# Optimization experiments

Measured on AMD Instinct MI355X. Metric: run time of the kernel, lower is better.

The kernel has to match this reference:

```python
import jax, jax.numpy as jnp
import numpy as np
import math

# gpt-oss style GQA dims
H, HKV, D = 64, 8, 64          # query heads, kv heads, head_dim
M = H // HKV                    # q_mult (queries per kv head)
D_MODEL = 2880
SLIDING_WINDOW = 128
SM_SCALE = 1.0 / math.sqrt(D)
NEG = -1e30


def _rope_cos_sin(T):
    # YaRN / NTK-by-parts rope (gpt-oss RotaryEmbedding) with
    # base=150000, initial_context_length=1024, scaling=32, alpha=1, beta=32
    base, init_ctx, scaling, alpha, beta = 150000.0, 1024.0, 32.0, 1.0, 32.0
    d_half = D // 2
    freq = base ** (np.arange(0, D, 2, dtype=np.float32) / D)
    concentration = 0.1 * math.log(scaling) + 1.0
    low = d_half * math.log(init_ctx / (beta * 2.0 * math.pi)) / math.log(base)
    high = d_half * math.log(init_ctx / (alpha * 2.0 * math.pi)) / math.log(base)
    ramp = np.clip((np.arange(d_half, dtype=np.float32) - low) / (high - low), 0.0, 1.0)
    inv_freq = ramp / (scaling * freq) + (1.0 - ramp) / freq  # interp<->extrap blend
    freqs = np.outer(np.arange(T, dtype=np.float32), inv_freq)  # (T, D/2)
    return (jnp.asarray(np.cos(freqs) * concentration),
            jnp.asarray(np.sin(freqs) * concentration))


def _apply_rope(x, cos, sin):
    # x[..., :D/2], x[..., D/2:] rotated pairwise; cos/sin broadcast over head dims
    x1, x2 = jnp.split(x, 2, axis=-1)
    return jnp.concatenate([x1 * cos - x2 * sin, x2 * cos + x1 * sin], axis=-1)


def setup_inputs() -> dict:
    key = jax.random.key(0)
    ks = jax.random.split(key, 6)
    x = jax.random.normal(ks[0], (1, 1536, D_MODEL), dtype=jnp.float32)
    qkv_dim = D * (H + 2 * HKV)
    W_qkv = jax.random.normal(ks[1], (D_MODEL, qkv_dim), dtype=jnp.float32) * 0.02
    b_qkv = jax.random.normal(ks[2], (qkv_dim,), dtype=jnp.float32) * 0.02
    W_out = jax.random.normal(ks[3], (H * D, D_MODEL), dtype=jnp.float32) * 0.02
    b_out = jax.random.normal(ks[4], (D_MODEL,), dtype=jnp.float32) * 0.02
    sinks = jax.random.normal(ks[5], (H,), dtype=jnp.float32) / math.sqrt(D)
    return {"x": x, "W_qkv": W_qkv, "b_qkv": b_qkv, "W_out": W_out,
            "b_out": b_out, "sinks": sinks}


def reference(x, W_qkv, b_qkv, W_out, b_out, sinks):
    B, T, _ = x.shape
    qkv = x @ W_qkv + b_qkv
    q = qkv[..., :H * D].reshape(B, T, HKV, M, D)
    k = qkv[..., H * D:(H + HKV) * D].reshape(B, T, HKV, D)
    v = qkv[..., (H + HKV) * D:].reshape(B, T, HKV, D)
    cos, sin = _rope_cos_sin(T)
    q = _apply_rope(q, cos[None, :, None, None, :], sin[None, :, None, None, :])
    k = _apply_rope(k, cos[None, :, None, :], sin[None, :, None, :])
    # GQA scores: (B, HKV, M, Tq, Tk)
    logits = jnp.einsum('bqhmd,bkhd->bhmqk', q, k) * SM_SCALE
    i = jnp.arange(T)[:, None]
    j = jnp.arange(T)[None, :]
    mask = (j <= i) & (j > i - SLIDING_WINDOW)  # causal + sliding window
    logits = jnp.where(mask[None, None, None], logits, NEG)
    m = jnp.max(logits, axis=-1, keepdims=True)
    e = jnp.exp(logits - m)
    # learned per-head sink logit folded into the softmax denominator
    exp_sink = jnp.exp(sinks.reshape(HKV, M)[None, :, :, None, None] - m)
    w = e / (jnp.sum(e, axis=-1, keepdims=True) + exp_sink)
    out = jnp.einsum('bhmqk,bkhd->bqhmd', w, v).reshape(B, T, H * D)
    return out @ W_out + b_out
```

## Files before the change

### kernel.cpp

```cpp
#include <hip/hip_runtime.h>

typedef __bf16 bf16_t;
typedef __bf16 bfrag8 __attribute__((ext_vector_type(8)));
typedef float f32x4 __attribute__((ext_vector_type(4)));

#define T_SEQ 1536
#define LDQKV 5120
#define SM_SCALE 0.125f
#define LOG2E 1.4426950408889634f

__device__ __forceinline__ unsigned short b2u(bf16_t h) {
  union { bf16_t h; unsigned short u; } c; c.h = h; return c.u;
}
__device__ __forceinline__ unsigned int pack2(float lo, float hi) {
  return (unsigned int)b2u((bf16_t)lo) | ((unsigned int)b2u((bf16_t)hi) << 16);
}
__device__ __forceinline__ void gload_lds16(const bf16_t* g, bf16_t* l) {
  __builtin_amdgcn_global_load_lds(
      (const __attribute__((address_space(1))) void*)g,
      (__attribute__((address_space(3))) void*)l, 16, 0, 0);
}

__global__ __launch_bounds__(256, 3)
void gemm_bt(const bf16_t* __restrict__ A, const bf16_t* __restrict__ Bt,
             const float* __restrict__ bias, void* __restrict__ C,
             int M, int N, int K, int out_mode) {
  __shared__ __align__(16) bf16_t As[128 * 64];
  __shared__ __align__(16) bf16_t Bs[128 * 64];
  const int tid = threadIdx.x;
  const int wave = tid >> 6;
  const int lane = tid & 63;
  const int g = lane >> 4;
  const int lm = lane & 15;

  const int NX = gridDim.x;
  const int nwg = NX * gridDim.y;
  const int orig = blockIdx.y * NX + blockIdx.x;
  const int qq = nwg >> 3, rr = nwg & 7;
  const int xcd = orig & 7, sidx = orig >> 3;
  const int swz = (xcd < rr ? xcd * (qq + 1) : rr * (qq + 1) + (xcd - rr) * qq) + sidx;
  const int n0 = (swz % NX) * 128;
  const int m0 = (swz / NX) * 128;

  const int tot = K >> 6;
  const int KS = gridDim.z;
  const int s = blockIdx.z;
  const int base = tot / KS, rem = tot % KS;
  const int ksteps = base + (s < rem ? 1 : 0);
  const int kbeg = s * base + (s < rem ? s : rem);

  const int wm = (wave >> 1) * 64;
  const int wn = (wave & 1) * 64;
  const int srow = lane >> 3;
  const int sseg = lane & 7;
  const int sswz = sseg ^ srow;

  const bf16_t* gA = A + (size_t)(m0 + wave * 32 + srow) * K + sswz * 8;
  const bf16_t* gB = Bt + (size_t)(n0 + wave * 32 + srow) * K + sswz * 8;
  bf16_t* lA = As + (wave * 32) * 64;
  bf16_t* lB = Bs + (wave * 32) * 64;

  const f32x4 fz = {0.f, 0.f, 0.f, 0.f};
  f32x4 acc[4][4];
#pragma unroll
  for (int i = 0; i < 4; ++i)
#pragma unroll
    for (int j = 0; j < 4; ++j) acc[i][j] = fz;

  const int lm7 = lm & 7;
  for (int t = 0; t < ksteps; ++t) {
    const int k0 = (kbeg + t) << 6;
#pragma unroll
    for (int it = 0; it < 4; ++it) {
      gload_lds16(gA + (size_t)(it * 8) * K + k0, lA + it * 8 * 64);
      gload_lds16(gB + (size_t)(it * 8) * K + k0, lB + it * 8 * 64);
    }
    __syncthreads();
#pragma unroll
    for (int ks = 0; ks < 2; ++ks) {
      bfrag8 af[4], bfr[4];
#pragma unroll
      for (int i = 0; i < 4; ++i) {
        const int cA = ((ks * 4 + g) ^ lm7) * 8;
        af[i]  = *(const bfrag8*)(As + (wm + i * 16 + lm) * 64 + cA);
        bfr[i] = *(const bfrag8*)(Bs + (wn + i * 16 + lm) * 64 + cA);
      }
#pragma unroll
      for (int i = 0; i < 4; ++i)
#pragma unroll
        for (int j = 0; j < 4; ++j)
          acc[i][j] = __builtin_amdgcn_mfma_f32_16x16x32_bf16(af[i], bfr[j],
                                                              acc[i][j], 0, 0, 0);
    }
    __syncthreads();
  }

  float* Cpart = (float*)C + (out_mode == 2 ? (size_t)s * M * N : 0);
#pragma unroll
  for (int j = 0; j < 4; ++j) {
    int n = n0 + wn + j * 16 + lm;
    if (n >= N) continue;
    float bv = (out_mode == 2) ? 0.f : bias[n];
#pragma unroll
    for (int i = 0; i < 4; ++i) {
      int mr = m0 + wm + i * 16 + g * 4;
#pragma unroll
      for (int r = 0; r < 4; ++r) {
        float v = acc[i][j][r] + bv;
        size_t off = (size_t)(mr + r) * N + n;
        if (out_mode == 1) ((bf16_t*)C)[off] = (bf16_t)v;
        else               Cpart[off] = v;
      }
    }
  }
}

__global__ __launch_bounds__(256)
void reduce_splits(const float* __restrict__ p, size_t MN,
                   const float* __restrict__ bias, int N,
                   void* __restrict__ dst, int out_bf16, int nsplit) {
  const size_t i4 = ((size_t)blockIdx.x * 256 + threadIdx.x) * 4;
  const int col = (int)(i4 % (size_t)N);
  f32x4 v = *(const f32x4*)(bias + col);
  for (int s = 0; s < nsplit; ++s) {
    f32x4 a = *(const f32x4*)(p + (size_t)s * MN + i4);
#pragma unroll
    for (int e = 0; e < 4; ++e) v[e] += a[e];
  }
  if (out_bf16) {
    uint2 w;
    w.x = pack2(v[0], v[1]);
    w.y = pack2(v[2], v[3]);
    *(uint2*)((bf16_t*)dst + i4) = w;
  } else {
    *(f32x4*)((float*)dst + i4) = v;
  }
}

__global__ __launch_bounds__(256)
void convert_x(const float* __restrict__ src, bf16_t* __restrict__ dst) {
  const int i8 = (blockIdx.x * 256 + threadIdx.x) * 8;
  f32x4 a = *(const f32x4*)(src + i8);
  f32x4 b = *(const f32x4*)(src + i8 + 4);
  uint4 w;
  w.x = pack2(a[0], a[1]);
  w.y = pack2(a[2], a[3]);
  w.z = pack2(b[0], b[1]);
  w.w = pack2(b[2], b[3]);
  *(uint4*)(dst + i8) = w;
}

__global__ __launch_bounds__(256)
void transpose_w(const float* __restrict__ src, bf16_t* __restrict__ dst,
                 int Ksrc, int Nsrc) {
  __shared__ bf16_t tile[32 * 33];
  const int t = threadIdx.x;
  const int r = t >> 3;
  const int c4 = (t & 7) * 4;
  const int n0 = blockIdx.x * 32;
  const int k0 = blockIdx.y * 32;
  f32x4 v = {0.f, 0.f, 0.f, 0.f};
  if (n0 + c4 < Nsrc)
    v = *(const f32x4*)(src + (size_t)(k0 + r) * Nsrc + n0 + c4);
#pragma unroll
  for (int e = 0; e < 4; ++e) tile[(c4 + e) * 33 + r] = (bf16_t)v[e];
  __syncthreads();
  uint2 w;
  w.x = pack2((float)tile[r * 33 + c4], (float)tile[r * 33 + c4 + 1]);
  w.y = pack2((float)tile[r * 33 + c4 + 2], (float)tile[r * 33 + c4 + 3]);
  *(uint2*)(dst + (size_t)(n0 + r) * Ksrc + k0 + c4) = w;
}

__global__ __launch_bounds__(256, 2)
void gemm_mfma(const void* __restrict__ A, const float* __restrict__ B,
               const float* __restrict__ bias, void* __restrict__ C,
               int M, int N, int K, int a_bf16, int out_bf16) {
  __shared__ __align__(16) bf16_t As[128 * 64];
  __shared__ __align__(16) bf16_t Bs[128 * 72];
  const int tid = threadIdx.x;
  const int wave = tid >> 6;
  const int lane = tid & 63;
  const int g = lane >> 4;
  const int lm = lane & 15;
  const int m0 = blockIdx.y * 128;
  const int n0 = blockIdx.x * 128;
  const int wm = (wave >> 1) * 64;
  const int wn = (wave & 1) * 64;
  const int sr = lane >> 3;
  const int seg = lane & 7;
  const int pairk = tid & 31;
  const int cg = tid >> 5;

  int cb = n0 + cg * 16;
  if (cb > N - 16) cb = N - 16;

  const f32x4 fz = {0.f, 0.f, 0.f, 0.f};
  f32x4 acc[4][4];
#pragma unroll
  for (int i = 0; i < 4; ++i)
#pragma unroll
    for (int j = 0; j < 4; ++j) acc[i][j] = fz;

  for (int k0 = 0; k0 < K; k0 += 64) {
    bfrag8 areg[4];
    if (a_bf16) {
#pragma unroll
      for (int it = 0; it < 4; ++it) {
        int ra = (wave * 4 + it) * 8 + sr;
        areg[it] = *(const bfrag8*)((const bf16_t*)A + (size_t)(m0 + ra) * K + k0 + seg * 8);
      }
    } else {
#pragma unroll
      for (int it = 0; it < 4; ++it) {
        int ra = (wave * 4 + it) * 8 + sr;
        const float* ga = (const float*)A + (size_t)(m0 + ra) * K + k0 + seg * 8;
        f32x4 a0 = *(const f32x4*)ga;
        f32x4 a1 = *(const f32x4*)(ga + 4);
#pragma unroll
        for (int e = 0; e < 4; ++e) {
          areg[it][e]     = (bf16_t)a0[e];
          areg[it][e + 4] = (bf16_t)a1[e];
        }
      }
    }
    int kk = 2 * pairk;
    unsigned int pk[16];
    {
      const float* b0 = B + (size_t)(k0 + kk) * N + cb;
      const float* b1 = B + (size_t)(k0 + kk + 1) * N + cb;
      f32x4 x0 = *(const f32x4*)(b0),     x1 = *(const f32x4*)(b0 + 4);
      f32x4 x2 = *(const f32x4*)(b0 + 8), x3 = *(const f32x4*)(b0 + 12);
      f32x4 y0 = *(const f32x4*)(b1),     y1 = *(const f32x4*)(b1 + 4);
      f32x4 y2 = *(const f32x4*)(b1 + 8), y3 = *(const f32x4*)(b1 + 12);
#pragma unroll
      for (int e = 0; e < 4; ++e) {
        pk[e]      = pack2(x0[e], y0[e]);
        pk[e + 4]  = pack2(x1[e], y1[e]);
        pk[e + 8]  = pack2(x2[e], y2[e]);
        pk[e + 12] = pack2(x3[e], y3[e]);
      }
    }
    __syncthreads();
#pragma unroll
    for (int it = 0; it < 4; ++it) {
      int ra = (wave * 4 + it) * 8 + sr;
      *(bfrag8*)(As + ra * 64 + seg * 8) = areg[it];
    }
#pragma unroll
    for (int n = 0; n < 16; ++n)
      *(unsigned int*)(Bs + (cg * 16 + n) * 72 + kk) = pk[n];
    __syncthreads();
#pragma unroll
    for (int ks = 0; ks < 2; ++ks) {
      bfrag8 af[4], bfr[4];
#pragma unroll
      for (int i = 0; i < 4; ++i) {
        af[i]  = *(const bfrag8*)(As + (wm + i * 16 + lm) * 64 + ks * 32 + g * 8);
        bfr[i] = *(const bfrag8*)(Bs + (wn + i * 16 + lm) * 72 + ks * 32 + g * 8);
      }
#pragma unroll
      for (int i = 0; i < 4; ++i)
#pragma unroll
        for (int j = 0; j < 4; ++j)
          acc[i][j] = __builtin_amdgcn_mfma_f32_16x16x32_bf16(af[i], bfr[j],
                                                              acc[i][j], 0, 0, 0);
    }
  }
#pragma unroll
  for (int j = 0; j < 4; ++j) {
    int n = n0 + wn + j * 16 + lm;
    if (n >= N) continue;
    float bv = bias[n];
#pragma unroll
    for (int i = 0; i < 4; ++i) {
      int mr = m0 + wm + i * 16 + g * 4;
#pragma unroll
      for (int r = 0; r < 4; ++r) {
        float v = acc[i][j][r] + bv;
        size_t off = (size_t)(mr + r) * N + n;
        if (out_bf16) ((bf16_t*)C)[off] = (bf16_t)v;
        else          ((float*)C)[off] = v;
      }
    }
  }
}

__global__ __launch_bounds__(256)
void rope_kernel(bf16_t* __restrict__ qkv) {
  int idx = blockIdx.x * 256 + threadIdx.x;
  int d = idx & 31;
  int rest = idx >> 5;
  int u = rest % 72;
  int t = rest / 72;
  if (t >= T_SEQ) return;
  int col = (u < 64) ? (u * 64) : (4096 + (u - 64) * 64);
  size_t off = (size_t)t * LDQKV + col + d;
  float x1 = (float)qkv[off];
  float x2 = (float)qkv[off + 32];
  const float lowv = 4.370846f;
  const float highv = 13.675927f;
  const float conc = 1.3465736f;
  float ramp = ((float)d - lowv) / (highv - lowv);
  ramp = fminf(fmaxf(ramp, 0.f), 1.f);
  float freq = exp2f((float)d * 0.53733134f);
  float inv_freq = ramp / (32.f * freq) + (1.f - ramp) / freq;
  float ang = (float)t * inv_freq;
  float c = cosf(ang) * conc;
  float s = sinf(ang) * conc;
  qkv[off]      = (bf16_t)(x1 * c - x2 * s);
  qkv[off + 32] = (bf16_t)(x2 * c + x1 * s);
}

__global__ __launch_bounds__(256, 2)
void attn_mfma(const bf16_t* __restrict__ qkv, const float* __restrict__ sinks,
               bf16_t* __restrict__ attno) {
  __shared__ __align__(16) bf16_t Vt[64 * 40];
  const int tid = threadIdx.x;
  const int wave = tid >> 6;
  const int lane = tid & 63;
  const int g = lane >> 4;
  const int lm = lane & 15;
  const int q0 = blockIdx.x * 32;
  const int kvh = blockIdx.y;
  const int jbase = q0 - 128;
  const int kt0 = (blockIdx.x < 4) ? (4 - blockIdx.x) : 0;

  bfrag8 qf[4][2];
#pragma unroll
  for (int nq = 0; nq < 4; ++nq) {
    const int h = 2 * wave + (nq >> 1);
    const int qr = q0 + (nq & 1) * 16 + lm;
    const bf16_t* qp = qkv + (size_t)qr * LDQKV + kvh * 512 + h * 64 + g * 8;
    qf[nq][0] = *(const bfrag8*)qp;
    qf[nq][1] = *(const bfrag8*)(qp + 32);
  }

  const f32x4 fz = {0.f, 0.f, 0.f, 0.f};
  f32x4 ot[4][4];
#pragma unroll
  for (int dt = 0; dt < 4; ++dt)
#pragma unroll
    for (int nq = 0; nq < 4; ++nq) ot[dt][nq] = fz;
  float mrow[4] = {-1e30f, -1e30f, -1e30f, -1e30f};
  float lrow[4] = {0.f, 0.f, 0.f, 0.f};

  const int vj = tid >> 3;
  const int vd = (tid & 7) * 8;

  for (int kt = kt0; kt < 5; ++kt) {
    const int ktb = jbase + kt * 32;
    __syncthreads();
    {
      bfrag8 v8 = *(const bfrag8*)(qkv + (size_t)(ktb + vj) * LDQKV + 4608 + kvh * 64 + vd);
#pragma unroll
      for (int e = 0; e < 8; ++e) Vt[(vd + e) * 40 + vj] = v8[e];
    }
    bfrag8 kf[2][2];
#pragma unroll
    for (int nk = 0; nk < 2; ++nk) {
      const bf16_t* kp = qkv + (size_t)(ktb + nk * 16 + lm) * LDQKV + 4096 + kvh * 64 + g * 8;
      kf[nk][0] = *(const bfrag8*)kp;
      kf[nk][1] = *(const bfrag8*)(kp + 32);
    }
    f32x4 st[2][4];
#pragma unroll
    for (int nk = 0; nk < 2; ++nk)
#pragma unroll
      for (int nq = 0; nq < 4; ++nq) st[nk][nq] = fz;
#pragma unroll
    for (int ks = 0; ks < 2; ++ks)
#pragma unroll
      for (int nk = 0; nk < 2; ++nk)
#pragma unroll
        for (int nq = 0; nq < 4; ++nq)
          st[nk][nq] = __builtin_amdgcn_mfma_f32_16x16x32_bf16(
              kf[nk][ks], qf[nq][ks], st[nk][nq], 0, 0, 0);

    bfrag8 paf[4];
#pragma unroll
    for (int nq = 0; nq < 4; ++nq) {
      const int q = q0 + (nq & 1) * 16 + lm;
      float sc[8];
      float pm = -1e30f;
#pragma unroll
      for (int nk = 0; nk < 2; ++nk)
#pragma unroll
        for (int r = 0; r < 4; ++r) {
          const int j = ktb + nk * 16 + g * 4 + r;
          const bool ok = (j <= q) && (j > q - 128);
          const float s = ok ? st[nk][nq][r] * (SM_SCALE * LOG2E) : -1e30f;
          sc[nk * 4 + r] = s;
          pm = fmaxf(pm, s);
        }
      pm = fmaxf(pm, __shfl_xor(pm, 16));
      pm = fmaxf(pm, __shfl_xor(pm, 32));
      const float mn = fmaxf(mrow[nq], pm);
      const float alpha = exp2f(mrow[nq] - mn);
      mrow[nq] = mn;
      float p[8];
      float ls = 0.f;
#pragma unroll
      for (int e = 0; e < 8; ++e) {
        p[e] = (sc[e] > -1e29f) ? exp2f(sc[e] - mn) : 0.f;
        ls += p[e];
      }
      lrow[nq] = lrow[nq] * alpha + ls;
#pragma unroll
      for (int dt = 0; dt < 4; ++dt) ot[dt][nq] *= alpha;
      unsigned pk00 = pack2(p[0], p[1]);
      unsigned pk01 = pack2(p[2], p[3]);
      unsigned pk10 = pack2(p[4], p[5]);
      unsigned pk11 = pack2(p[6], p[7]);
      const int srcA = ((g & 1) << 5) | lm;
      const int srcB = srcA + 16;
      unsigned a0 = __shfl(pk00, srcA), b0 = __shfl(pk10, srcA);
      unsigned a1 = __shfl(pk01, srcA), b1 = __shfl(pk11, srcA);
      unsigned a2 = __shfl(pk00, srcB), b2 = __shfl(pk10, srcB);
      unsigned a3 = __shfl(pk01, srcB), b3 = __shfl(pk11, srcB);
      const bool hiw = g >= 2;
      union { unsigned u[4]; bfrag8 f; } pa;
      pa.u[0] = hiw ? b0 : a0;
      pa.u[1] = hiw ? b1 : a1;
      pa.u[2] = hiw ? b2 : a2;
      pa.u[3] = hiw ? b3 : a3;
      paf[nq] = pa.f;
    }
    __syncthreads();
#pragma unroll
    for (int dt = 0; dt < 4; ++dt) {
      const bfrag8 vtf = *(const bfrag8*)(Vt + (dt * 16 + lm) * 40 + g * 8);
#pragma unroll
      for (int nq = 0; nq < 4; ++nq)
        ot[dt][nq] = __builtin_amdgcn_mfma_f32_16x16x32_bf16(
            vtf, paf[nq], ot[dt][nq], 0, 0, 0);
    }
  }

#pragma unroll
  for (int nq = 0; nq < 4; ++nq) {
    float lt = lrow[nq] + __shfl_xor(lrow[nq], 16);
    lt += __shfl_xor(lt, 32);
    const int h = 2 * wave + (nq >> 1);
    const float sk = sinks[kvh * 8 + h];
    const float inv = 1.f / (lt + exp2f(sk * LOG2E - mrow[nq]));
    const int q = q0 + (nq & 1) * 16 + lm;
    bf16_t* op = attno + (size_t)q * 4096 + kvh * 512 + h * 64;
#pragma unroll
    for (int dt = 0; dt < 4; ++dt) {
      const f32x4 o = ot[dt][nq];
      uint2 w;
      w.x = pack2(o[0] * inv, o[1] * inv);
      w.y = pack2(o[2] * inv, o[3] * inv);
      *(uint2*)(op + dt * 16 + g * 4) = w;
    }
  }
}

__global__ __launch_bounds__(256)
void sentinel_fill(float* __restrict__ out, int n) {
  int i = blockIdx.x * 256 + threadIdx.x;
  if (i < n) out[i] = 10000.0f;
}

extern "C" void kernel_launch(void* const* d_in, const int* in_sizes, int n_in,
                              void* d_out, int out_size, void* d_ws, size_t ws_size,
                              hipStream_t stream) {
  const float *x = nullptr, *Wqkv = nullptr, *bqkv = nullptr,
              *Wout = nullptr, *bout = nullptr, *sinks = nullptr;
  for (int i = 0; i < n_in; ++i) {
    switch (in_sizes[i]) {
      case 1536 * 2880:  x = (const float*)d_in[i]; break;
      case 2880 * 5120:  Wqkv = (const float*)d_in[i]; break;
      case 5120:         bqkv = (const float*)d_in[i]; break;
      case 4096 * 2880:  Wout = (const float*)d_in[i]; break;
      case 2880:         bout = (const float*)d_in[i]; break;
      case 64:           sinks = (const float*)d_in[i]; break;
      default: break;
    }
  }

  const size_t N_QKV  = (size_t)1536 * 5120;
  const size_t N_ATT  = (size_t)1536 * 4096;
  const size_t N_XB   = (size_t)1536 * 2880;
  const size_t N_WQT  = (size_t)5120 * 2880;
  const size_t N_WOT  = (size_t)2944 * 4096;
  const size_t REQ_OLD = (N_QKV + N_ATT) * sizeof(bf16_t);
  const size_t REQ_BIG = (N_QKV + N_ATT + N_XB + N_WQT + N_WOT) * sizeof(bf16_t);
  const size_t REQ_SPLIT2 = REQ_BIG + 2 * N_QKV * sizeof(float);
  const size_t REQ_SPLIT3 = REQ_BIG + 3 * N_QKV * sizeof(float);

  if (ws_size < REQ_OLD || !x || !Wqkv || !bqkv || !Wout || !bout || !sinks) {
    sentinel_fill<<<(out_size + 255) / 256, 256, 0, stream>>>((float*)d_out, out_size);
    return;
  }

  bf16_t* qkv   = (bf16_t*)d_ws;
  bf16_t* attno = qkv + N_QKV;

  if (ws_size >= REQ_BIG) {
    bf16_t* xb  = attno + N_ATT;
    bf16_t* WqT = xb + N_XB;
    bf16_t* WoT = WqT + N_WQT;
    convert_x<<<2160, 256, 0, stream>>>(x, xb);
    transpose_w<<<dim3(160, 90), 256, 0, stream>>>(Wqkv, WqT, 2880, 5120);
    transpose_w<<<dim3(92, 128), 256, 0, stream>>>(Wout, WoT, 4096, 2880);

    if (ws_size >= REQ_SPLIT2) {
      const int ks1 = (ws_size >= REQ_SPLIT3) ? 3 : 2;
      const int ks2 = (ws_size >= REQ_SPLIT3) ? 4 : 2;
      float* part = (float*)(WoT + N_WOT);
      gemm_bt<<<dim3(40, 12, ks1), 256, 0, stream>>>(
          xb, WqT, nullptr, part, 1536, 5120, 2880, 2);
      reduce_splits<<<7680, 256, 0, stream>>>(part, N_QKV, bqkv, 5120, qkv, 1, ks1);
      rope_kernel<<<dim3((1536 * 72 * 32) / 256), 256, 0, stream>>>(qkv);
      attn_mfma<<<dim3(1536 / 32, 8), 256, 0, stream>>>(qkv, sinks, attno);
      gemm_bt<<<dim3(23, 12, ks2), 256, 0, stream>>>(
          attno, WoT, nullptr, part, 1536, 2880, 4096, 2);
      reduce_splits<<<4320, 256, 0, stream>>>(part, N_XB, bout, 2880, d_out, 0, ks2);
    } else {
      gemm_bt<<<dim3(40, 12, 1), 256, 0, stream>>>(xb, WqT, bqkv, qkv,
                                                   1536, 5120, 2880, 1);
      rope_kernel<<<dim3((1536 * 72 * 32) / 256), 256, 0, stream>>>(qkv);
      attn_mfma<<<dim3(1536 / 32, 8), 256, 0, stream>>>(qkv, sinks, attno);
      gemm_bt<<<dim3(23, 12, 1), 256, 0, stream>>>(attno, WoT, bout, d_out,
                                                   1536, 2880, 4096, 0);
    }
  } else {
    gemm_mfma<<<dim3(5120 / 128, 1536 / 128), 256, 0, stream>>>(
        x, Wqkv, bqkv, qkv, 1536, 5120, 2880, 0, 1);
    rope_kernel<<<dim3((1536 * 72 * 32) / 256), 256, 0, stream>>>(qkv);
    attn_mfma<<<dim3(1536 / 32, 8), 256, 0, stream>>>(qkv, sinks, attno);
    gemm_mfma<<<dim3((2880 + 127) / 128, 1536 / 128), 256, 0, stream>>>(
        attno, Wout, bout, d_out, 1536, 2880, 4096, 1, 0);
  }
}
```

Baseline: 359.4 us.

## Double-buffer GEMM LDS tiles and fuse RoPE into unsplit QKV GEMM epilogue

Result: slower. 698.8 us (+94.4%).

```diff
diff --git a/kernel.cpp b/kernel.cpp
--- a/kernel.cpp
+++ b/kernel.cpp
@@ -21,12 +21,12 @@
       (__attribute__((address_space(3))) void*)l, 16, 0, 0);
 }
 
-__global__ __launch_bounds__(256, 3)
+__global__ __launch_bounds__(256, 2)
 void gemm_bt(const bf16_t* __restrict__ A, const bf16_t* __restrict__ Bt,
              const float* __restrict__ bias, void* __restrict__ C,
-             int M, int N, int K, int out_mode) {
-  __shared__ __align__(16) bf16_t As[128 * 64];
-  __shared__ __align__(16) bf16_t Bs[128 * 64];
+             int M, int N, int K, int out_mode, int do_rope) {
+  __shared__ __align__(16) bf16_t As[2][128 * 64];
+  __shared__ __align__(16) bf16_t Bs[2][128 * 64];
   const int tid = threadIdx.x;
   const int wave = tid >> 6;
   const int lane = tid & 63;
@@ -57,8 +57,6 @@
 
   const bf16_t* gA = A + (size_t)(m0 + wave * 32 + srow) * K + sswz * 8;
   const bf16_t* gB = Bt + (size_t)(n0 + wave * 32 + srow) * K + sswz * 8;
-  bf16_t* lA = As + (wave * 32) * 64;
-  bf16_t* lB = Bs + (wave * 32) * 64;
 
   const f32x4 fz = {0.f, 0.f, 0.f, 0.f};
   f32x4 acc[4][4];
@@ -67,23 +65,34 @@
 #pragma unroll
     for (int j = 0; j < 4; ++j) acc[i][j] = fz;
 
+#define STAGE_TILE(b, tt)                                                      \
+  {                                                                            \
+    const int k0s = (kbeg + (tt)) << 6;                                        \
+    _Pragma("unroll")                                                          \
+    for (int it = 0; it < 4; ++it) {                                           \
+      gload_lds16(gA + (size_t)(it * 8) * K + k0s,                             \
+                  &As[b][(wave * 32 + it * 8) * 64]);                          \
+      gload_lds16(gB + (size_t)(it * 8) * K + k0s,                             \
+                  &Bs[b][(wave * 32 + it * 8) * 64]);                          \
+    }                                                                          \
+  }
+
   const int lm7 = lm & 7;
+  STAGE_TILE(0, 0);
+  __syncthreads();
+  int cur = 0;
   for (int t = 0; t < ksteps; ++t) {
-    const int k0 = (kbeg + t) << 6;
-#pragma unroll
-    for (int it = 0; it < 4; ++it) {
-      gload_lds16(gA + (size_t)(it * 8) * K + k0, lA + it * 8 * 64);
-      gload_lds16(gB + (size_t)(it * 8) * K + k0, lB + it * 8 * 64);
-    }
-    __syncthreads();
+    if (t + 1 < ksteps) {
+      if (cur) STAGE_TILE(0, t + 1) else STAGE_TILE(1, t + 1);
+    }
 #pragma unroll
     for (int ks = 0; ks < 2; ++ks) {
       bfrag8 af[4], bfr[4];
 #pragma unroll
       for (int i = 0; i < 4; ++i) {
         const int cA = ((ks * 4 + g) ^ lm7) * 8;
-        af[i]  = *(const bfrag8*)(As + (wm + i * 16 + lm) * 64 + cA);
-        bfr[i] = *(const bfrag8*)(Bs + (wn + i * 16 + lm) * 64 + cA);
+        af[i]  = *(const bfrag8*)(&As[cur][(wm + i * 16 + lm) * 64 + cA]);
+        bfr[i] = *(const bfrag8*)(&Bs[cur][(wn + i * 16 + lm) * 64 + cA]);
       }
 #pragma unroll
       for (int i = 0; i < 4; ++i)
@@ -93,8 +102,42 @@
                                                               acc[i][j], 0, 0, 0);
     }
     __syncthreads();
-  }
-
+    cur ^= 1;
+  }
+#undef STAGE_TILE
+
+  if (do_rope && out_mode == 1 && n0 + wn < 4608) {
+    const float lowv = 4.370846f;
+    const float highv = 13.675927f;
+    const float conc = 1.3465736f;
+#pragma unroll
+    for (int j = 0; j < 2; ++j) {
+      const int n = n0 + wn + j * 16 + lm;
+      const float bv1 = bias[n];
+      const float bv2 = bias[n + 32];
+      const float d = (float)(j * 16 + lm);
+      float ramp = (d - lowv) / (highv - lowv);
+      ramp = fminf(fmaxf(ramp, 0.f), 1.f);
+      const float freq = exp2f(d * 0.53733134f);
+      const float inv_freq = ramp / (32.f * freq) + (1.f - ramp) / freq;
+#pragma unroll
+      for (int i = 0; i < 4; ++i) {
+        const int mr = m0 + wm + i * 16 + g * 4;
+#pragma unroll
+        for (int r = 0; r < 4; ++r) {
+          const float ang = (float)(mr + r) * inv_freq;
+          const float c = cosf(ang) * conc;
+          const float sn = sinf(ang) * conc;
+          const float x1 = acc[i][j][r] + bv1;
+          const float x2 = acc[i][j + 2][r] + bv2;
+          const size_t off = (size_t)(mr + r) * N + n;
+          ((bf16_t*)C)[off]      = (bf16_t)(x1 * c - x2 * sn);
+          ((bf16_t*)C)[off + 32] = (bf16_t)(x2 * c + x1 * sn);
+        }
+      }
+    }
+    return;
+  }
   float* Cpart = (float*)C + (out_mode == 2 ? (size_t)s * M * N : 0);
 #pragma unroll
   for (int j = 0; j < 4; ++j) {
@@ -486,8 +529,7 @@
   const size_t N_WOT  = (size_t)2944 * 4096;
   const size_t REQ_OLD = (N_QKV + N_ATT) * sizeof(bf16_t);
   const size_t REQ_BIG = (N_QKV + N_ATT + N_XB + N_WQT + N_WOT) * sizeof(bf16_t);
-  const size_t REQ_SPLIT2 = REQ_BIG + 2 * N_QKV * sizeof(float);
-  const size_t REQ_SPLIT3 = REQ_BIG + 3 * N_QKV * sizeof(float);
+  const size_t REQ_G2 = REQ_BIG + 2 * N_XB * sizeof(float);
 
   if (ws_size < REQ_OLD || !x || !Wqkv || !bqkv || !Wout || !bout || !sinks) {
     sentinel_fill<<<(out_size + 255) / 256, 256, 0, stream>>>((float*)d_out, out_size);
@@ -505,25 +547,18 @@
     transpose_w<<<dim3(160, 90), 256, 0, stream>>>(Wqkv, WqT, 2880, 5120);
     transpose_w<<<dim3(92, 128), 256, 0, stream>>>(Wout, WoT, 4096, 2880);
 
-    if (ws_size >= REQ_SPLIT2) {
-      const int ks1 = (ws_size >= REQ_SPLIT3) ? 3 : 2;
-      const int ks2 = (ws_size >= REQ_SPLIT3) ? 4 : 2;
+    gemm_bt<<<dim3(40, 12, 1), 256, 0, stream>>>(
+        xb, WqT, bqkv, qkv, 1536, 5120, 2880, 1, 1);
+    attn_mfma<<<dim3(1536 / 32, 8), 256, 0, stream>>>(qkv, sinks, attno);
+
+    if (ws_size >= REQ_G2) {
       float* part = (float*)(WoT + N_WOT);
-      gemm_bt<<<dim3(40, 12, ks1), 256, 0, stream>>>(
-          xb, WqT, nullptr, part, 1536, 5120, 2880, 2);
-      reduce_splits<<<7680, 256, 0, stream>>>(part, N_QKV, bqkv, 5120, qkv, 1, ks1);
-      rope_kernel<<<dim3((1536 * 72 * 32) / 256), 256, 0, stream>>>(qkv);
-      attn_mfma<<<dim3(1536 / 32, 8), 256, 0, stream>>>(qkv, sinks, attno);
-      gemm_bt<<<dim3(23, 12, ks2), 256, 0, stream>>>(
-          attno, WoT, nullptr, part, 1536, 2880, 4096, 2);
-      reduce_splits<<<4320, 256, 0, stream>>>(part, N_XB, bout, 2880, d_out, 0, ks2);
+      gemm_bt<<<dim3(23, 12, 2), 256, 0, stream>>>(
+          attno, WoT, nullptr, part, 1536, 2880, 4096, 2, 0);
+      reduce_splits<<<4320, 256, 0, stream>>>(part, N_XB, bout, 2880, d_out, 0, 2);
     } else {
-      gemm_bt<<<dim3(40, 12, 1), 256, 0, stream>>>(xb, WqT, bqkv, qkv,
-                                                   1536, 5120, 2880, 1);
-      rope_kernel<<<dim3((1536 * 72 * 32) / 256), 256, 0, stream>>>(qkv);
-      attn_mfma<<<dim3(1536 / 32, 8), 256, 0, stream>>>(qkv, sinks, attno);
-      gemm_bt<<<dim3(23, 12, 1), 256, 0, stream>>>(attno, WoT, bout, d_out,
-                                                   1536, 2880, 4096, 0);
+      gemm_bt<<<dim3(23, 12, 1), 256, 0, stream>>>(
+          attno, WoT, bout, d_out, 1536, 2880, 4096, 0, 0);
     }
   } else {
     gemm_mfma<<<dim3(5120 / 128, 1536 / 128), 256, 0, stream>>>(
```

## Fuse split-K reduction with RoPE and fix split factor at two

Applied to the files above, without the earlier changes.

Measured after the change: 332.5 us. -7.5%, faster.

```diff
diff --git a/kernel.cpp b/kernel.cpp
--- a/kernel.cpp
+++ b/kernel.cpp
@@ -113,6 +113,55 @@
       }
     }
   }
+}
+
+__global__ __launch_bounds__(256)
+void reduce_rope(const float* __restrict__ p, size_t MN,
+                 const float* __restrict__ bias,
+                 bf16_t* __restrict__ qkv, int nsplit) {
+  const int idx = blockIdx.x * 256 + threadIdx.x;
+  const int qd = idx & 7;
+  const int rest = idx >> 3;
+  const int u = rest % 80;
+  const int t = rest / 80;
+  const int c = u * 64 + qd * 4;
+  const size_t off = (size_t)t * LDQKV + c;
+  f32x4 lo = *(const f32x4*)(bias + c);
+  f32x4 hi = *(const f32x4*)(bias + c + 32);
+  for (int s = 0; s < nsplit; ++s) {
+    const float* ps = p + (size_t)s * MN + off;
+    f32x4 a = *(const f32x4*)ps;
+    f32x4 b = *(const f32x4*)(ps + 32);
+#pragma unroll
+    for (int e = 0; e < 4; ++e) { lo[e] += a[e]; hi[e] += b[e]; }
+  }
+  uint2 wlo, whi;
+  if (u < 72) {
+    const float lowv = 4.370846f;
+    const float highv = 13.675927f;
+    const float conc = 1.3465736f;
+    float olo[4], ohi[4];
+#pragma unroll
+    for (int e = 0; e < 4; ++e) {
+      const float d = (float)(qd * 4 + e);
+      float ramp = (d - lowv) / (highv - lowv);
+      ramp = fminf(fmaxf(ramp, 0.f), 1.f);
+      const float freq = exp2f(d * 0.53733134f);
+      const float inv_freq = ramp / (32.f * freq) + (1.f - ramp) / freq;
+      const float ang = (float)t * inv_freq;
+      const float cs = cosf(ang) * conc;
+      const float sn = sinf(ang) * conc;
+      olo[e] = lo[e] * cs - hi[e] * sn;
+      ohi[e] = hi[e] * cs + lo[e] * sn;
+    }
+    wlo.x = pack2(olo[0], olo[1]); wlo.y = pack2(olo[2], olo[3]);
+    whi.x = pack2(ohi[0], ohi[1]); whi.y = pack2(ohi[2], ohi[3]);
+  } else {
+    wlo.x = pack2(lo[0], lo[1]); wlo.y = pack2(lo[2], lo[3]);
+    whi.x = pack2(hi[0], hi[1]); whi.y = pack2(hi[2], hi[3]);
+  }
+  *(uint2*)(qkv + off) = wlo;
+  *(uint2*)(qkv + off + 32) = whi;
 }
 
 __global__ __launch_bounds__(256)
@@ -487,7 +536,6 @@
   const size_t REQ_OLD = (N_QKV + N_ATT) * sizeof(bf16_t);
   const size_t REQ_BIG = (N_QKV + N_ATT + N_XB + N_WQT + N_WOT) * sizeof(bf16_t);
   const size_t REQ_SPLIT2 = REQ_BIG + 2 * N_QKV * sizeof(float);
-  const size_t REQ_SPLIT3 = REQ_BIG + 3 * N_QKV * sizeof(float);
 
   if (ws_size < REQ_OLD || !x || !Wqkv || !bqkv || !Wout || !bout || !sinks) {
     sentinel_fill<<<(out_size + 255) / 256, 256, 0, stream>>>((float*)d_out, out_size);
@@ -506,17 +554,15 @@
     transpose_w<<<dim3(92, 128), 256, 0, stream>>>(Wout, WoT, 4096, 2880);
 
     if (ws_size >= REQ_SPLIT2) {
-      const int ks1 = (ws_size >= REQ_SPLIT3) ? 3 : 2;
-      const int ks2 = (ws_size >= REQ_SPLIT3) ? 4 : 2;
       float* part = (float*)(WoT + N_WOT);
-      gemm_bt<<<dim3(40, 12, ks1), 256, 0, stream>>>(
+      gemm_bt<<<dim3(40, 12, 2), 256, 0, stream>>>(
           xb, WqT, nullptr, part, 1536, 5120, 2880, 2);
-      reduce_splits<<<7680, 256, 0, stream>>>(part, N_QKV, bqkv, 5120, qkv, 1, ks1);
-      rope_kernel<<<dim3((1536 * 72 * 32) / 256), 256, 0, stream>>>(qkv);
+      reduce_rope<<<(1536 * 80 * 8) / 256, 256, 0, stream>>>(
+          part, N_QKV, bqkv, qkv, 2);
       attn_mfma<<<dim3(1536 / 32, 8), 256, 0, stream>>>(qkv, sinks, attno);
-      gemm_bt<<<dim3(23, 12, ks2), 256, 0, stream>>>(
+      gemm_bt<<<dim3(23, 12, 2), 256, 0, stream>>>(
           attno, WoT, nullptr, part, 1536, 2880, 4096, 2);
-      reduce_splits<<<4320, 256, 0, stream>>>(part, N_XB, bout, 2880, d_out, 0, ks2);
+      reduce_splits<<<4320, 256, 0, stream>>>(part, N_XB, bout, 2880, d_out, 0, 2);
     } else {
       gemm_bt<<<dim3(40, 12, 1), 256, 0, stream>>>(xb, WqT, bqkv, qkv,
                                                    1536, 5120, 2880, 1);
```
